# Performance work log

Measured on AMD Instinct MI355X. Metric: run time of the kernel, lower is better.

Reference implementation:

```python
import jax, jax.numpy as jnp
import numpy as np

B, T = 16, 2048
D_MODEL, D_INNER, D_STATE, D_CONV, DT_RANK = 64, 128, 16, 4, 4

def leaky(x):
    return jnp.where(x >= 0, x, 0.01 * x)

def silu(x):
    return x * jax.nn.sigmoid(x)

def conv1d(x, w, b, pad):
    # x: (b,c,t), w: (o,i,k)
    y = jax.lax.conv_general_dilated(x, w, (1,), [(pad, pad)],
        dimension_numbers=('NCH', 'OIH', 'NCH'))
    return y + b[None, :, None]

def pixel_shuffle_1d(x, r):
    b, cr, t = x.shape
    c = cr // r
    return x.reshape(b, c, r, t).transpose(0, 1, 3, 2).reshape(b, c, t * r)

def rmsnorm(x, w, eps=1e-5):
    return x * jax.lax.rsqrt(jnp.mean(x * x, -1, keepdims=True) + eps) * w

def batchnorm(x, g, b, eps=1e-5):
    # training-mode BatchNorm1d: stats over (N, T) per channel
    mu = jnp.mean(x, axis=(0, 2), keepdims=True)
    var = jnp.var(x, axis=(0, 2), keepdims=True)
    return (x - mu) * jax.lax.rsqrt(var + eps) * g[None, :, None] + b[None, :, None]

def selective_scan(u, delta, A, Bm, Cm, D):
    # u, delta: (b,t,d); Bm, Cm: (b,t,n); A: (d,n); D: (d,)
    def step(h, inp):
        d_t, u_t, B_t, C_t = inp  # (b,d),(b,d),(b,n),(b,n)
        dA = jnp.exp(d_t[:, :, None] * A[None])              # (b,d,n)
        h = h * dA + (d_t * u_t)[:, :, None] * B_t[:, None, :]
        y = jnp.einsum('bdn,bn->bd', h, C_t)
        return h, y
    h0 = jnp.zeros((u.shape[0], A.shape[0], A.shape[1]), u.dtype)
    xs = tuple(jnp.swapaxes(a, 0, 1) for a in (delta, u, Bm, Cm))
    _, ys = jax.lax.scan(step, h0, xs)
    return jnp.swapaxes(ys, 0, 1) + u * D[None, None, :]

def mamba_layer(x, norm_w, in_proj_w, dwconv_w, dwconv_b, x_proj_w,
                dt_proj_w, dt_proj_b, A_log, D, out_proj_w):
    # x: (b,t,d_model); pre-norm residual Mamba block
    xn = rmsnorm(x, norm_w)
    xz = xn @ in_proj_w.T                                    # (b,t,2*d_inner)
    xm, z = jnp.split(xz, 2, axis=-1)
    # causal depthwise conv over time (pad left d_conv-1)
    xc = jax.lax.conv_general_dilated(jnp.swapaxes(xm, 1, 2), dwconv_w,
        (1,), [(D_CONV - 1, 0)], dimension_numbers=('NCH', 'OIH', 'NCH'),
        feature_group_count=D_INNER) + dwconv_b[None, :, None]
    xm = silu(jnp.swapaxes(xc, 1, 2))                        # (b,t,d_inner)
    x_dbl = xm @ x_proj_w.T                                  # (b,t,dt_rank+2n)
    dt, Bm, Cm = jnp.split(x_dbl, [DT_RANK, DT_RANK + D_STATE], axis=-1)
    delta = jax.nn.softplus(dt @ dt_proj_w.T + dt_proj_b)    # (b,t,d_inner)
    A = -jnp.exp(A_log)                                      # (d_inner,n)
    y = selective_scan(xm, delta, A, Bm, Cm, D)
    y = y * silu(z)
    return x + y @ out_proj_w.T

def setup_inputs():
    key = jax.random.key(0)
    ks = jax.random.split(key, 16)
    p = lambda k, shp, s=0.02: jax.random.normal(k, shp, jnp.float32) * s
    return {
        'x': jax.random.normal(ks[0], (B, 12, T), jnp.float32),
        'conv_in_w': p(ks[1], (D_MODEL, 12, 15)), 'conv_in_b': jnp.zeros((D_MODEL,), jnp.float32),
        'norm_w': jnp.ones((D_MODEL,), jnp.float32),
        'in_proj_w': p(ks[2], (2 * D_INNER, D_MODEL)),
        'dwconv_w': p(ks[3], (D_INNER, 1, D_CONV), 0.2), 'dwconv_b': jnp.zeros((D_INNER,), jnp.float32),
        'x_proj_w': p(ks[4], (DT_RANK + 2 * D_STATE, D_INNER)),
        'dt_proj_w': p(ks[5], (D_INNER, DT_RANK), 0.5),
        'dt_proj_b': jnp.full((D_INNER,), -2.0, jnp.float32),
        'A_log': jnp.tile(jnp.log(jnp.arange(1, D_STATE + 1, dtype=jnp.float32))[None], (D_INNER, 1)),
        'D': jnp.ones((D_INNER,), jnp.float32),
        'out_proj_w': p(ks[6], (D_MODEL, D_INNER)),
        'merge_w': p(ks[7], (D_MODEL, D_MODEL, 15)), 'merge_b': jnp.zeros((D_MODEL,), jnp.float32),
        'bn_g': jnp.ones((D_MODEL,), jnp.float32), 'bn_b': jnp.zeros((D_MODEL,), jnp.float32),
        'up1_w': p(ks[8], (320 * 5, D_MODEL, 15)), 'up1_b': jnp.zeros((320 * 5,), jnp.float32),
        'up2_w': p(ks[9], (128 * 2, 320, 15)), 'up2_b': jnp.zeros((128 * 2,), jnp.float32),
        'out_w': p(ks[10], (12, 128, 15)), 'out_b': jnp.zeros((12,), jnp.float32),
    }

def reference(x, conv_in_w, conv_in_b, norm_w, in_proj_w, dwconv_w, dwconv_b,
              x_proj_w, dt_proj_w, dt_proj_b, A_log, D, out_proj_w,
              merge_w, merge_b, bn_g, bn_b, up1_w, up1_b, up2_w, up2_b,
              out_w, out_b):
    h = leaky(conv1d(x, conv_in_w, conv_in_b, 7))            # (b,64,t)
    hold = h
    s = mamba_layer(jnp.swapaxes(h, 1, 2), norm_w, in_proj_w, dwconv_w,
                    dwconv_b, x_proj_w, dt_proj_w, dt_proj_b, A_log, D,
                    out_proj_w)
    h2 = jnp.swapaxes(s, 1, 2)                               # (b,64,t)
    m = batchnorm(conv1d(h2, merge_w, merge_b, 7), bn_g, bn_b) + hold
    u5 = leaky(pixel_shuffle_1d(conv1d(m, up1_w, up1_b, 7), 5))    # (b,320,5t)
    u10 = leaky(pixel_shuffle_1d(conv1d(u5, up2_w, up2_b, 7), 2))  # (b,128,10t)
    return conv1d(u10, out_w, out_b, 7)                      # (b,12,10t)
```

## Files before the change

### kernel.cpp

```cpp
#include <hip/hip_runtime.h>
#include <hip/hip_bf16.h>
#include <math.h>

typedef __hip_bfloat16 bf16;
typedef __attribute__((ext_vector_type(8))) short short8;
typedef __attribute__((ext_vector_type(4))) float f32x4;

#define BB 16
#define TT 2048
#define DM 64
#define DI 128
#define DSN 16
#define NCHK 32
#define CLEN 64

union U8 { int4 i4; unsigned short u[8]; };

__device__ __forceinline__ bf16  f2b(float v){ return __float2bfloat16(v); }
__device__ __forceinline__ float b2f(bf16 v){ return __bfloat162float(v); }
__device__ __forceinline__ unsigned short f2bu(float v){
  bf16 b = __float2bfloat16(v); unsigned short u; __builtin_memcpy(&u,&b,2); return u;
}
__device__ __forceinline__ float bu2f(unsigned short u){
  unsigned int x = ((unsigned int)u) << 16; float f; __builtin_memcpy(&f,&x,4); return f;
}
__device__ __forceinline__ float siluf(float x){ return x / (1.f + __expf(-x)); }
__device__ __forceinline__ float leakyf(float x){ return x >= 0.f ? x : 0.01f*x; }
__device__ __forceinline__ float softplusf(float x){ return x > 20.f ? x : log1pf(__expf(x)); }

__global__ __launch_bounds__(256) void k_zero(float* __restrict__ p, int n){
  int i = blockIdx.x*256 + threadIdx.x;
  if (i < n) p[i] = 0.f;
}

__global__ __launch_bounds__(256) void k_pack(
    const float* __restrict__ w, short* __restrict__ wp,
    int COUT, int CIN, int NTg, int NCH, int NTAP)
{
  int i = blockIdx.x*256 + threadIdx.x;
  int lane = i & 63, frag = i >> 6;
  int total = NTAP*NCH*NTg;
  if (frag >= total) return;
  int cot = frag % NTg; int kc = frag / NTg;
  int ch = kc % NCH;    int k  = kc / NCH;
  int co = cot*16 + (lane & 15);
  int ci0 = ch*32 + (lane >> 4)*8;
  unsigned short v[8];
  #pragma unroll
  for (int j = 0; j < 8; j++)
    v[j] = (co < COUT) ? f2bu(w[((size_t)co*CIN + ci0 + j)*NTAP + k]) : (unsigned short)0;
  short* dst = wp + (size_t)frag*512 + lane*8;
  *(int4*)dst = *(int4*)v;
}

__global__ __launch_bounds__(256) void k_conv_in(
    const float* __restrict__ x, const float* __restrict__ w,
    const float* __restrict__ bias, float* __restrict__ h, bf16* __restrict__ ht)
{
  __shared__ float sx[12][272];
  __shared__ float sw[12][15];
  int tid = threadIdx.x;
  int t0 = blockIdx.x * 256;
  int co = blockIdx.y;
  int b  = blockIdx.z;
  for (int i = tid; i < 12*15; i += 256) sw[i/15][i%15] = w[co*180 + i];
  for (int i = tid; i < 12*270; i += 256) {
    int ci = i/270, L = i%270;
    int tt = t0 - 7 + L;
    sx[ci][L] = (tt >= 0 && tt < TT) ? x[((size_t)b*12+ci)*TT + tt] : 0.f;
  }
  __syncthreads();
  float acc = bias[co];
  #pragma unroll
  for (int ci = 0; ci < 12; ci++) {
    #pragma unroll
    for (int k = 0; k < 15; k++)
      acc += sx[ci][tid+k]*sw[ci][k];
  }
  acc = leakyf(acc);
  int t = t0 + tid;
  h [((size_t)b*DM + co)*TT + t] = acc;
  ht[((size_t)b*TT + t)*DM + co] = f2b(acc);
}

__global__ __launch_bounds__(256) void k_inproj_mfma(
    const bf16* __restrict__ ht, const float* __restrict__ nw,
    const short* __restrict__ wp, bf16* __restrict__ xm, bf16* __restrict__ z)
{
  __shared__ short sxa[64*128];
  __shared__ float sred[64][4];
  const int tid = threadIdx.x;
  const int lane = tid & 63, wv = tid >> 6;
  const int lnm = lane & 15, quad = lane >> 4;
  const size_t bt0 = (size_t)blockIdx.x * 64;

  {
    int row = tid >> 2, part = tid & 3, ch0 = part*16;
    const short* src = (const short*)ht + (bt0 + row)*64 + ch0;
    U8 p0, p1; p0.i4 = *(const int4*)src; p1.i4 = *(const int4*)(src + 8);
    float f[16]; float ss = 0.f;
    #pragma unroll
    for (int j = 0; j < 8; j++) { f[j] = bu2f(p0.u[j]); f[8+j] = bu2f(p1.u[j]); }
    #pragma unroll
    for (int j = 0; j < 16; j++) ss += f[j]*f[j];
    sred[row][part] = ss;
    __syncthreads();
    float tot = sred[row][0]+sred[row][1]+sred[row][2]+sred[row][3];
    float sc = rsqrtf(tot*(1.f/64.f) + 1e-5f);
    U8 o0, o1;
    #pragma unroll
    for (int j = 0; j < 8; j++) {
      o0.u[j] = f2bu(f[j]  *sc*nw[ch0+j]);
      o1.u[j] = f2bu(f[8+j]*sc*nw[ch0+8+j]);
    }
    int s0 = part*2, s1 = part*2+1;
    *(int4*)(sxa + row*128 + ((s0 ^ (row&7))<<3)) = o0.i4;
    *(int4*)(sxa + row*128 + ((s1 ^ (row&7))<<3)) = o1.i4;
  }
  __syncthreads();

  f32x4 acc[4][4];
  #pragma unroll
  for (int m = 0; m < 4; m++)
    #pragma unroll
    for (int n = 0; n < 4; n++) acc[m][n] = (f32x4){0.f,0.f,0.f,0.f};

  #pragma unroll
  for (int kc = 0; kc < 2; kc++) {
    short8 bfr[4];
    #pragma unroll
    for (int n = 0; n < 4; n++) {
      int fid = kc*16 + wv*4 + n;
      bfr[n] = *(const short8*)(wp + (size_t)fid*512 + lane*8);
    }
    #pragma unroll
    for (int m = 0; m < 4; m++) {
      int r2 = m*16 + lnm;
      short8 a = *(const short8*)(sxa + r2*128 + (((kc*4+quad) ^ (r2&7))<<3));
      #pragma unroll
      for (int n = 0; n < 4; n++)
        acc[m][n] = __builtin_amdgcn_mfma_f32_16x16x32_bf16(a, bfr[n], acc[m][n], 0, 0, 0);
    }
  }

  #pragma unroll
  for (int m = 0; m < 4; m++)
    #pragma unroll
    for (int n = 0; n < 4; n++) {
      int co = wv*64 + n*16 + lnm;
      float v[4] = {acc[m][n].x, acc[m][n].y, acc[m][n].z, acc[m][n].w};
      #pragma unroll
      for (int r = 0; r < 4; r++) {
        size_t t = bt0 + m*16 + quad*4 + r;
        if (co < 128) xm[t*128 + co]       = f2b(v[r]);
        else          z [t*128 + (co-128)] = f2b(v[r]);
      }
    }
}

__global__ __launch_bounds__(256) void k_dwconv(
    const bf16* __restrict__ xm, const float* __restrict__ w,
    const float* __restrict__ bias, float* __restrict__ xcf, bf16* __restrict__ xcb)
{
  int idx = blockIdx.x*256 + threadIdx.x;
  int c = idx & (DI-1);
  int bt = idx >> 7;
  int t = bt & (TT-1);
  float acc = bias[c];
  #pragma unroll
  for (int k = 0; k < 4; k++) {
    int tt = t - 3 + k;
    if (tt >= 0) acc += b2f(xm[(size_t)(bt - 3 + k)*DI + c]) * w[c*4+k];
  }
  float v = siluf(acc);
  xcf[idx] = v;
  xcb[idx] = f2b(v);
}

__global__ __launch_bounds__(256) void k_xproj_mfma(
    const bf16* __restrict__ xcb, const short* __restrict__ wp, float* __restrict__ xd)
{
  __shared__ __align__(16) char smem[256*64];
  const int tid = threadIdx.x;
  const int lane = tid & 63, wv = tid >> 6;
  const int lnm = lane & 15, quad = lane >> 4;
  const size_t bt0 = (size_t)blockIdx.x * 256;
  const int wvt = wv*64;

  f32x4 acc[4][3];
  #pragma unroll
  for (int m = 0; m < 4; m++)
    #pragma unroll
    for (int n = 0; n < 3; n++) acc[m][n] = (f32x4){0.f,0.f,0.f,0.f};

  for (int ch = 0; ch < 4; ch++) {
    __syncthreads();
    int sl = tid & 3;
    for (int r = tid >> 2; r < 256; r += 64) {
      int4 v = *(const int4*)((const short*)xcb + (bt0 + r)*128 + ch*32 + sl*8);
      *(int4*)(&smem[r*64 + ((sl ^ (r & 3)) << 4)]) = v;
    }
    __syncthreads();
    short8 bfr[3];
    #pragma unroll
    for (int n = 0; n < 3; n++)
      bfr[n] = *(const short8*)(wp + (size_t)(ch*3+n)*512 + lane*8);
    #pragma unroll
    for (int m = 0; m < 4; m++) {
      int row = wvt + m*16 + lnm;
      short8 a = *(const short8*)(&smem[row*64 + ((quad ^ (row & 3)) << 4)]);
      #pragma unroll
      for (int n = 0; n < 3; n++)
        acc[m][n] = __builtin_amdgcn_mfma_f32_16x16x32_bf16(a, bfr[n], acc[m][n], 0, 0, 0);
    }
  }
  #pragma unroll
  for (int m = 0; m < 4; m++)
    #pragma unroll
    for (int n = 0; n < 3; n++) {
      int cho = n*16 + lnm;
      float v[4] = {acc[m][n].x, acc[m][n].y, acc[m][n].z, acc[m][n].w};
      #pragma unroll
      for (int r = 0; r < 4; r++) {
        size_t t = bt0 + wvt + m*16 + quad*4 + r;
        xd[t*48 + cho] = v[r];
      }
    }
}

__global__ __launch_bounds__(256) void k_delta(
    const float* __restrict__ xd, const float* __restrict__ w,
    const float* __restrict__ bias, float* __restrict__ dlt)
{
  int idx = blockIdx.x*256 + threadIdx.x;
  int c = idx & (DI-1);
  int bt = idx >> 7;
  const float* dt = xd + (size_t)bt*48;
  float acc = bias[c];
  #pragma unroll
  for (int r = 0; r < 4; r++) acc += dt[r]*w[c*4+r];
  dlt[idx] = softplusf(acc);
}

__global__ __launch_bounds__(256) void k_scan_sum(
    const float* __restrict__ dlt, const float* __restrict__ xcf,
    const float* __restrict__ xd, const float* __restrict__ A_log,
    float* __restrict__ gP, float* __restrict__ gS)
{
  int tid = threadIdx.x;
  int n = tid & 15, dl = tid >> 4;
  int d = blockIdx.x*16 + dl;
  int b = blockIdx.y, ck = blockIdx.z;
  float A = -__expf(A_log[d*DSN + n]);
  float P = 1.f, h = 0.f;
  size_t base = (size_t)b*TT + (size_t)ck*CLEN;
  for (int i = 0; i < CLEN; i++) {
    size_t ib = base + i;
    float dd = dlt[ib*DI + d];
    float uu = xcf[ib*DI + d];
    float Bv = xd [ib*48 + 4 + n];
    float dA = __expf(dd*A);
    h = h*dA + dd*uu*Bv;
    P *= dA;
  }
  size_t idx = (((size_t)b*NCHK + ck)*DI + d)*DSN + n;
  gP[idx] = P; gS[idx] = h;
}

__global__ __launch_bounds__(256) void k_scan_comb(
    const float* __restrict__ gP, const float* __restrict__ gS,
    float* __restrict__ ghs)
{
  int idx = blockIdx.x*256 + threadIdx.x;
  int n = idx & 15, d = (idx >> 4) & 127, b = idx >> 11;
  float h = 0.f;
  for (int c = 0; c < NCHK; c++) {
    size_t j = (((size_t)b*NCHK + c)*DI + d)*DSN + n;
    ghs[j] = h;
    h = gP[j]*h + gS[j];
  }
}

__global__ __launch_bounds__(256) void k_scan_out(
    const float* __restrict__ dlt, const float* __restrict__ xcf,
    const float* __restrict__ xd, const float* __restrict__ A_log,
    const float* __restrict__ Dv, const float* __restrict__ ghs,
    float* __restrict__ y)
{
  int tid = threadIdx.x;
  int n = tid & 15, dl = tid >> 4;
  int d = blockIdx.x*16 + dl;
  int b = blockIdx.y, ck = blockIdx.z;
  float A = -__expf(A_log[d*DSN + n]);
  float Dd = Dv[d];
  size_t idx = (((size_t)b*NCHK + ck)*DI + d)*DSN + n;
  float h = ghs[idx];
  size_t base = (size_t)b*TT + (size_t)ck*CLEN;
  for (int i = 0; i < CLEN; i++) {
    size_t ib = base + i;
    float dd = dlt[ib*DI + d];
    float uu = xcf[ib*DI + d];
    float Bv = xd [ib*48 + 4  + n];
    float Cv = xd [ib*48 + 20 + n];
    float dA = __expf(dd*A);
    h = h*dA + dd*uu*Bv;
    float c = h*Cv;
    c += __shfl_xor(c, 1); c += __shfl_xor(c, 2);
    c += __shfl_xor(c, 4); c += __shfl_xor(c, 8);
    if (n == 0) y[ib*DI + d] = c + uu*Dd;
  }
}

__global__ __launch_bounds__(256) void k_outproj_mfma(
    const float* __restrict__ gy, const bf16* __restrict__ gz,
    const bf16* __restrict__ ht, const short* __restrict__ wp,
    bf16* __restrict__ st)
{
  __shared__ __align__(16) char smem[256*64];
  const int tid = threadIdx.x;
  const int lane = tid & 63, wv = tid >> 6;
  const int lnm = lane & 15, quad = lane >> 4;
  const size_t bt0 = (size_t)blockIdx.x * 256;
  const int wvt = wv*64;

  f32x4 acc[4][4];
  #pragma unroll
  for (int m = 0; m < 4; m++)
    #pragma unroll
    for (int n = 0; n < 4; n++) acc[m][n] = (f32x4){0.f,0.f,0.f,0.f};

  for (int ch = 0; ch < 4; ch++) {
    __syncthreads();
    int sl = tid & 3;
    for (int r = tid >> 2; r < 256; r += 64) {
      size_t base = (bt0 + r)*(size_t)DI + ch*32 + sl*8;
      float4 y0 = *(const float4*)(gy + base);
      float4 y1 = *(const float4*)(gy + base + 4);
      U8 zz; zz.i4 = *(const int4*)((const short*)gz + base);
      float yv[8] = {y0.x, y0.y, y0.z, y0.w, y1.x, y1.y, y1.z, y1.w};
      U8 o;
      #pragma unroll
      for (int j = 0; j < 8; j++)
        o.u[j] = f2bu(yv[j] * siluf(bu2f(zz.u[j])));
      *(int4*)(&smem[r*64 + ((sl ^ (r & 3)) << 4)]) = o.i4;
    }
    __syncthreads();
    short8 bfr[4];
    #pragma unroll
    for (int n = 0; n < 4; n++)
      bfr[n] = *(const short8*)(wp + (size_t)(ch*4+n)*512 + lane*8);
    #pragma unroll
    for (int m = 0; m < 4; m++) {
      int row = wvt + m*16 + lnm;
      short8 a = *(const short8*)(&smem[row*64 + ((quad ^ (row & 3)) << 4)]);
      #pragma unroll
      for (int n = 0; n < 4; n++)
        acc[m][n] = __builtin_amdgcn_mfma_f32_16x16x32_bf16(a, bfr[n], acc[m][n], 0, 0, 0);
    }
  }
  #pragma unroll
  for (int m = 0; m < 4; m++)
    #pragma unroll
    for (int n = 0; n < 4; n++) {
      int cho = n*16 + lnm;
      float v[4] = {acc[m][n].x, acc[m][n].y, acc[m][n].z, acc[m][n].w};
      #pragma unroll
      for (int r = 0; r < 4; r++) {
        size_t t = bt0 + wvt + m*16 + quad*4 + r;
        st[t*DM + cho] = f2b(v[r] + b2f(ht[t*DM + cho]));
      }
    }
}

template<int CIN, int NSUB, int R, bool LEAKY, bool STATS, int OUTMODE>
__global__ __launch_bounds__(256) void mfma_conv(
    const bf16* __restrict__ inp, const short* __restrict__ wp,
    const float* __restrict__ bias, void* __restrict__ outv,
    float* __restrict__ stats, int Tlen, int NTg)
{
  constexpr int NCH = CIN/32;
  constexpr int NC  = 16*NSUB;
  constexpr int NCR = NC/R;
  constexpr int STAGE_B = 270*64;
  constexpr int EPI_B = (OUTMODE==0) ? 4*64*NC*2 : 4*16*68*4;
  constexpr int LDSB = (STAGE_B > EPI_B) ? STAGE_B : EPI_B;
  __shared__ __align__(16) char smem[LDSB];

  const int tid  = threadIdx.x;
  const int lane = tid & 63;
  const int wv   = tid >> 6;
  const int lnm  = lane & 15;
  const int quad = lane >> 4;
  const int t0   = blockIdx.x * 256;
  const int by   = blockIdx.y;
  const int b    = blockIdx.z;
  const int wvt  = wv*64;

  f32x4 acc[4][NSUB];
  #pragma unroll
  for (int m = 0; m < 4; m++)
    #pragma unroll
    for (int n = 0; n < NSUB; n++)
      acc[m][n] = (f32x4){0.f,0.f,0.f,0.f};

  for (int ch = 0; ch < NCH; ch++) {
    __syncthreads();
    {
      int sl = tid & 3;
      for (int r = tid >> 2; r < 270; r += 64) {
        int t = t0 - 7 + r;
        int4 v = {0,0,0,0};
        if (t >= 0 && t < Tlen)
          v = *(const int4*)(inp + ((size_t)((size_t)b*Tlen + t))*CIN + ch*32 + sl*8);
        *(int4*)(&smem[r*64 + ((sl ^ (r & 3)) << 4)]) = v;
      }
    }
    __syncthreads();

    short8 bcur[NSUB], bnxt[NSUB];
    #pragma unroll
    for (int n = 0; n < NSUB; n++) {
      size_t fid = (size_t)((0*NCH + ch)*NTg + by*NSUB + n);
      bcur[n] = *(const short8*)(wp + fid*512 + lane*8);
    }
    for (int k = 0; k < 15; k++) {
      if (k < 14) {
        #pragma unroll
        for (int n = 0; n < NSUB; n++) {
          size_t fid = (size_t)(((k+1)*NCH + ch)*NTg + by*NSUB + n);
          bnxt[n] = *(const short8*)(wp + fid*512 + lane*8);
        }
      }
      short8 af[4];
      #pragma unroll
      for (int m = 0; m < 4; m++) {
        int row = wvt + m*16 + lnm + k;
        af[m] = *(const short8*)(&smem[row*64 + ((quad ^ (row & 3)) << 4)]);
      }
      #pragma unroll
      for (int m = 0; m < 4; m++)
        #pragma unroll
        for (int n = 0; n < NSUB; n++)
          acc[m][n] = __builtin_amdgcn_mfma_f32_16x16x32_bf16(af[m], bcur[n], acc[m][n], 0, 0, 0);
      #pragma unroll
      for (int n = 0; n < NSUB; n++) bcur[n] = bnxt[n];
    }
  }

  #pragma unroll
  for (int n = 0; n < NSUB; n++) {
    float bv = bias[by*NC + n*16 + lnm];
    #pragma unroll
    for (int m = 0; m < 4; m++) {
      acc[m][n].x += bv; acc[m][n].y += bv; acc[m][n].z += bv; acc[m][n].w += bv;
    }
  }
  if (STATS) {
    #pragma unroll
    for (int n = 0; n < NSUB; n++) {
      float s1 = 0.f, s2 = 0.f;
      #pragma unroll
      for (int m = 0; m < 4; m++) {
        f32x4 a = acc[m][n];
        s1 += a.x + a.y + a.z + a.w;
        s2 += a.x*a.x + a.y*a.y + a.z*a.z + a.w*a.w;
      }
      s1 += __shfl_xor(s1, 16); s1 += __shfl_xor(s1, 32);
      s2 += __shfl_xor(s2, 16); s2 += __shfl_xor(s2, 32);
      if (quad == 0) {
        atomicAdd(&stats[by*NC + n*16 + lnm], s1);
        atomicAdd(&stats[64 + by*NC + n*16 + lnm], s2);
      }
    }
  }
  if (LEAKY) {
    #pragma unroll
    for (int m = 0; m < 4; m++)
      #pragma unroll
      for (int n = 0; n < NSUB; n++) {
        acc[m][n].x = leakyf(acc[m][n].x); acc[m][n].y = leakyf(acc[m][n].y);
        acc[m][n].z = leakyf(acc[m][n].z); acc[m][n].w = leakyf(acc[m][n].w);
      }
  }

  __syncthreads();

  if (OUTMODE == 0) {
    short* Cw = (short*)smem + wv*64*NC;
    #pragma unroll
    for (int m = 0; m < 4; m++)
      #pragma unroll
      for (int n = 0; n < NSUB; n++) {
        int co = n*16 + lnm;
        int p = co % R, c = co / R;
        float vv[4] = {acc[m][n].x, acc[m][n].y, acc[m][n].z, acc[m][n].w};
        #pragma unroll
        for (int r = 0; r < 4; r++) {
          int t = m*16 + quad*4 + r;
          Cw[t*NC + p*NCR + c] = (short)f2bu(vv[r]);
        }
      }
    const int SPT = NC/8;
    const int CTOT = NTg*16/R;
    bf16* outp = (bf16*)outv;
    size_t brow = (size_t)b * ((size_t)Tlen*R);
    for (int j = lane; j < 64*SPT; j += 64) {
      int t = j / SPT, sl = j % SPT;
      int cosw = sl*8;
      int p = cosw / NCR, csl = cosw % NCR;
      int tout = (t0 + wvt + t)*R + p;
      size_t ga = (brow + tout)*(size_t)CTOT + (size_t)by*NCR + csl;
      *(int4*)((short*)outp + ga) = *(const int4*)(Cw + t*NC + cosw);
    }
  } else {
    float* Cw = (float*)smem + wv*(16*68);
    #pragma unroll
    for (int m = 0; m < 4; m++) {
      float vv[4] = {acc[m][0].x, acc[m][0].y, acc[m][0].z, acc[m][0].w};
      #pragma unroll
      for (int r = 0; r < 4; r++) {
        int t = m*16 + quad*4 + r;
        Cw[lnm*68 + t] = vv[r];
      }
    }
    float* outf = (float*)outv;
    for (int j = lane; j < 12*16; j += 64) {
      int co = j >> 4, t4 = (j & 15)*4;
      size_t ga = ((size_t)b*12 + co)*(size_t)Tlen + t0 + wvt + t4;
      *(float4*)(outf + ga) = *(const float4*)(Cw + co*68 + t4);
    }
  }
}

__global__ __launch_bounds__(256) void k_bnadd2(
    const bf16* __restrict__ m2, const float* __restrict__ stats,
    const float* __restrict__ g, const float* __restrict__ bb,
    const float* __restrict__ h, bf16* __restrict__ mt)
{
  int idx = blockIdx.x*256 + threadIdx.x;
  int c = idx & 63;
  int t = (idx >> 6) & (TT-1);
  int b = idx >> 17;
  const float cnt = (float)(BB*TT);
  float mu  = stats[c] / cnt;
  float var = stats[64+c] / cnt - mu*mu;
  float inv = rsqrtf(var + 1e-5f);
  float v = b2f(m2[idx]);
  float hv = h[((size_t)b*64 + c)*TT + t];
  mt[idx] = f2b((v - mu)*inv*g[c] + bb[c] + hv);
}

extern "C" void kernel_launch(void* const* d_in, const int* in_sizes, int n_in,
                              void* d_out, int out_size, void* d_ws, size_t ws_size,
                              hipStream_t stream)
{
  const float* in_x       = (const float*)d_in[0];
  const float* conv_in_w  = (const float*)d_in[1];
  const float* conv_in_b  = (const float*)d_in[2];
  const float* norm_w     = (const float*)d_in[3];
  const float* in_proj_w  = (const float*)d_in[4];
  const float* dwconv_w   = (const float*)d_in[5];
  const float* dwconv_b   = (const float*)d_in[6];
  const float* x_proj_w   = (const float*)d_in[7];
  const float* dt_proj_w  = (const float*)d_in[8];
  const float* dt_proj_b  = (const float*)d_in[9];
  const float* A_log      = (const float*)d_in[10];
  const float* Dvec       = (const float*)d_in[11];
  const float* out_proj_w = (const float*)d_in[12];
  const float* merge_w    = (const float*)d_in[13];
  const float* merge_b    = (const float*)d_in[14];
  const float* bn_g       = (const float*)d_in[15];
  const float* bn_b       = (const float*)d_in[16];
  const float* up1_w      = (const float*)d_in[17];
  const float* up1_b      = (const float*)d_in[18];
  const float* up2_w      = (const float*)d_in[19];
  const float* up2_b      = (const float*)d_in[20];
  const float* out_w      = (const float*)d_in[21];
  const float* out_b      = (const float*)d_in[22];
  float* out = (float*)d_out;

  size_t off = 0;
  auto take = [&](size_t bytes) -> void* {
    void* p = (char*)d_ws + off;
    off += (bytes + 255) & ~(size_t)255;
    return p;
  };
  const size_t F_BDMT = (size_t)BB*DM*TT;
  const size_t F_BTDI = (size_t)BB*TT*DI;
  float* g_h   = (float*)take(F_BDMT*4);
  bf16*  g_ht  = (bf16*) take(F_BDMT*2);
  bf16*  g_st  = (bf16*) take(F_BDMT*2);
  bf16*  g_m2  = (bf16*) take(F_BDMT*2);
  bf16*  g_mt  = (bf16*) take(F_BDMT*2);
  float* g_stt = (float*)take(512);
  short* wp_mg = (short*)take((size_t)15*2*4 *512*2);
  short* wp_u1 = (short*)take((size_t)15*2*100*512*2);
  short* wp_u2 = (short*)take((size_t)15*10*16*512*2);
  short* wp_oc = (short*)take((size_t)15*4*1  *512*2);
  short* wp_ip = (short*)take((size_t)1*2*16*512*2);
  short* wp_xp = (short*)take((size_t)1*4*3 *512*2);
  short* wp_op = (short*)take((size_t)1*4*4 *512*2);
  size_t mamba_base = off;
  bf16*  g_xm  = (bf16*) take(F_BTDI*2);
  bf16*  g_z   = (bf16*) take(F_BTDI*2);
  float* g_xcf = (float*)take(F_BTDI*4);
  bf16*  g_xcb = (bf16*) take(F_BTDI*2);
  float* g_xd  = (float*)take((size_t)BB*TT*48*4);
  float* g_dl  = (float*)take(F_BTDI*4);
  float* g_y   = (float*)take(F_BTDI*4);
  float* g_P   = (float*)take((size_t)BB*NCHK*DI*DSN*4);
  float* g_S   = (float*)take((size_t)BB*NCHK*DI*DSN*4);
  float* g_hs  = (float*)take((size_t)BB*NCHK*DI*DSN*4);
  bf16*  g_u10 = (bf16*)((char*)d_ws + mamba_base);
  bf16*  g_u5  = (bf16*)take((size_t)BB*10240*320*2);
  if (off > ws_size) return;

  k_zero<<<1, 256, 0, stream>>>(g_stt, 128);
  k_pack<<<(15*2*4*64+255)/256, 256, 0, stream>>>(merge_w, wp_mg, 64, 64, 4, 2, 15);
  k_pack<<<(15*2*100*64+255)/256, 256, 0, stream>>>(up1_w, wp_u1, 1600, 64, 100, 2, 15);
  k_pack<<<(15*10*16*64+255)/256, 256, 0, stream>>>(up2_w, wp_u2, 256, 320, 16, 10, 15);
  k_pack<<<(15*4*1*64+255)/256, 256, 0, stream>>>(out_w, wp_oc, 12, 128, 1, 4, 15);
  k_pack<<<(1*2*16*64+255)/256, 256, 0, stream>>>(in_proj_w, wp_ip, 256, 64, 16, 2, 1);
  k_pack<<<(1*4*3*64+255)/256, 256, 0, stream>>>(x_proj_w, wp_xp, 36, 128, 3, 4, 1);
  k_pack<<<(1*4*4*64+255)/256, 256, 0, stream>>>(out_proj_w, wp_op, 64, 128, 4, 4, 1);

  k_conv_in<<<dim3(TT/256, DM, BB), 256, 0, stream>>>(in_x, conv_in_w, conv_in_b, g_h, g_ht);

  k_inproj_mfma<<<BB*TT/64, 256, 0, stream>>>(g_ht, norm_w, wp_ip, g_xm, g_z);
  k_dwconv<<<BB*TT*DI/256, 256, 0, stream>>>(g_xm, dwconv_w, dwconv_b, g_xcf, g_xcb);
  k_xproj_mfma<<<BB*TT/256, 256, 0, stream>>>(g_xcb, wp_xp, g_xd);
  k_delta<<<BB*TT*DI/256, 256, 0, stream>>>(g_xd, dt_proj_w, dt_proj_b, g_dl);
  k_scan_sum<<<dim3(DI/16, BB, NCHK), 256, 0, stream>>>(g_dl, g_xcf, g_xd, A_log, g_P, g_S);
  k_scan_comb<<<BB*DI*DSN/256, 256, 0, stream>>>(g_P, g_S, g_hs);
  k_scan_out<<<dim3(DI/16, BB, NCHK), 256, 0, stream>>>(g_dl, g_xcf, g_xd, A_log, Dvec, g_hs, g_y);
  k_outproj_mfma<<<BB*TT/256, 256, 0, stream>>>(g_y, g_z, g_ht, wp_op, g_st);

  mfma_conv<64,4,1,false,true,0><<<dim3(TT/256, 1, BB), 256, 0, stream>>>(
      g_st, wp_mg, merge_b, g_m2, g_stt, TT, 4);
  k_bnadd2<<<BB*TT*64/256, 256, 0, stream>>>(g_m2, g_stt, bn_g, bn_b, g_h, g_mt);

  mfma_conv<64,5,5,true,false,0><<<dim3(TT/256, 20, BB), 256, 0, stream>>>(
      g_mt, wp_u1, up1_b, g_u5, nullptr, TT, 100);

  mfma_conv<320,4,2,true,false,0><<<dim3(TT*5/256, 4, BB), 256, 0, stream>>>(
      g_u5, wp_u2, up2_b, g_u10, nullptr, TT*5, 16);

  mfma_conv<128,1,1,false,false,1><<<dim3(TT*10/256, 1, BB), 256, 0, stream>>>(
      g_u10, wp_oc, out_b, out, nullptr, TT*10, 1);
}
```

Baseline: 889.2 us.

## Drop fp32 intermediates, widen conv LDS staging to 64 channels, double up2 N-tile

Removes the fp32 copies of the conv_in output and the dwconv output. The residual, the scan inputs and the scan output y are now read and written as bf16, which cuts global memory traffic across several Mamba kernels. The generic MFMA conv now stages 64 input channels per LDS pass with an 8-way swizzle, and it drops the register double-buffering of weight fragments. The up2 conv uses NSUB=8 with half as many grid blocks, and the epilogue is split into halves so the LDS budget holds. This adds bf16 rounding of the residual and of y, and the larger per-wave accumulator set may raise register pressure.

```diff
diff --git a/kernel.cpp b/kernel.cpp
--- a/kernel.cpp
+++ b/kernel.cpp
@@ -55,7 +55,7 @@
 
 __global__ __launch_bounds__(256) void k_conv_in(
     const float* __restrict__ x, const float* __restrict__ w,
-    const float* __restrict__ bias, float* __restrict__ h, bf16* __restrict__ ht)
+    const float* __restrict__ bias, bf16* __restrict__ ht)
 {
   __shared__ float sx[12][272];
   __shared__ float sw[12][15];
@@ -79,7 +79,6 @@
   }
   acc = leakyf(acc);
   int t = t0 + tid;
-  h [((size_t)b*DM + co)*TT + t] = acc;
   ht[((size_t)b*TT + t)*DM + co] = f2b(acc);
 }
 
@@ -160,7 +159,7 @@
 
 __global__ __launch_bounds__(256) void k_dwconv(
     const bf16* __restrict__ xm, const float* __restrict__ w,
-    const float* __restrict__ bias, float* __restrict__ xcf, bf16* __restrict__ xcb)
+    const float* __restrict__ bias, bf16* __restrict__ xcb)
 {
   int idx = blockIdx.x*256 + threadIdx.x;
   int c = idx & (DI-1);
@@ -172,9 +171,7 @@
     int tt = t - 3 + k;
     if (tt >= 0) acc += b2f(xm[(size_t)(bt - 3 + k)*DI + c]) * w[c*4+k];
   }
-  float v = siluf(acc);
-  xcf[idx] = v;
-  xcb[idx] = f2b(v);
+  xcb[idx] = f2b(siluf(acc));
 }
 
 __global__ __launch_bounds__(256) void k_xproj_mfma(
@@ -243,7 +240,7 @@
 }
 
 __global__ __launch_bounds__(256) void k_scan_sum(
-    const float* __restrict__ dlt, const float* __restrict__ xcf,
+    const float* __restrict__ dlt, const bf16* __restrict__ xcb,
     const float* __restrict__ xd, const float* __restrict__ A_log,
     float* __restrict__ gP, float* __restrict__ gS)
 {
@@ -257,7 +254,7 @@
   for (int i = 0; i < CLEN; i++) {
     size_t ib = base + i;
     float dd = dlt[ib*DI + d];
-    float uu = xcf[ib*DI + d];
+    float uu = b2f(xcb[ib*DI + d]);
     float Bv = xd [ib*48 + 4 + n];
     float dA = __expf(dd*A);
     h = h*dA + dd*uu*Bv;
@@ -282,10 +279,10 @@
 }
 
 __global__ __launch_bounds__(256) void k_scan_out(
-    const float* __restrict__ dlt, const float* __restrict__ xcf,
+    const float* __restrict__ dlt, const bf16* __restrict__ xcb,
     const float* __restrict__ xd, const float* __restrict__ A_log,
     const float* __restrict__ Dv, const float* __restrict__ ghs,
-    float* __restrict__ y)
+    bf16* __restrict__ y)
 {
   int tid = threadIdx.x;
   int n = tid & 15, dl = tid >> 4;
@@ -299,7 +296,7 @@
   for (int i = 0; i < CLEN; i++) {
     size_t ib = base + i;
     float dd = dlt[ib*DI + d];
-    float uu = xcf[ib*DI + d];
+    float uu = b2f(xcb[ib*DI + d]);
     float Bv = xd [ib*48 + 4  + n];
     float Cv = xd [ib*48 + 20 + n];
     float dA = __expf(dd*A);
@@ -307,12 +304,12 @@
     float c = h*Cv;
     c += __shfl_xor(c, 1); c += __shfl_xor(c, 2);
     c += __shfl_xor(c, 4); c += __shfl_xor(c, 8);
-    if (n == 0) y[ib*DI + d] = c + uu*Dd;
+    if (n == 0) y[ib*DI + d] = f2b(c + uu*Dd);
   }
 }
 
 __global__ __launch_bounds__(256) void k_outproj_mfma(
-    const float* __restrict__ gy, const bf16* __restrict__ gz,
+    const bf16* __restrict__ gy, const bf16* __restrict__ gz,
     const bf16* __restrict__ ht, const short* __restrict__ wp,
     bf16* __restrict__ st)
 {
@@ -334,14 +331,12 @@
     int sl = tid & 3;
     for (int r = tid >> 2; r < 256; r += 64) {
       size_t base = (bt0 + r)*(size_t)DI + ch*32 + sl*8;
-      float4 y0 = *(const float4*)(gy + base);
-      float4 y1 = *(const float4*)(gy + base + 4);
+      U8 yy; yy.i4 = *(const int4*)((const short*)gy + base);
       U8 zz; zz.i4 = *(const int4*)((const short*)gz + base);
-      float yv[8] = {y0.x, y0.y, y0.z, y0.w, y1.x, y1.y, y1.z, y1.w};
       U8 o;
       #pragma unroll
       for (int j = 0; j < 8; j++)
-        o.u[j] = f2bu(yv[j] * siluf(bu2f(zz.u[j])));
+        o.u[j] = f2bu(bu2f(yy.u[j]) * siluf(bu2f(zz.u[j])));
       *(int4*)(&smem[r*64 + ((sl ^ (r & 3)) << 4)]) = o.i4;
     }
     __syncthreads();
@@ -378,11 +373,16 @@
     const float* __restrict__ bias, void* __restrict__ outv,
     float* __restrict__ stats, int Tlen, int NTg)
 {
-  constexpr int NCH = CIN/32;
-  constexpr int NC  = 16*NSUB;
-  constexpr int NCR = NC/R;
-  constexpr int STAGE_B = 270*64;
-  constexpr int EPI_B = (OUTMODE==0) ? 4*64*NC*2 : 4*16*68*4;
+  constexpr int NCH64 = CIN/64;
+  constexpr int NCH32 = CIN/32;
+  constexpr int NC   = 16*NSUB;
+  constexpr int NCR  = NC/R;
+  constexpr int NHALF = (NC > 80) ? 2 : 1;
+  constexpr int NCh  = NC/NHALF;
+  constexpr int NCRh = NCR/NHALF;
+  constexpr int NSUBh = NSUB/NHALF;
+  constexpr int STAGE_B = 270*128;
+  constexpr int EPI_B = (OUTMODE==0) ? 4*64*NCh*2 : 4*16*68*4;
   constexpr int LDSB = (STAGE_B > EPI_B) ? STAGE_B : EPI_B;
   __shared__ __align__(16) char smem[LDSB];
 
@@ -403,47 +403,39 @@
     for (int n = 0; n < NSUB; n++)
       acc[m][n] = (f32x4){0.f,0.f,0.f,0.f};
 
-  for (int ch = 0; ch < NCH; ch++) {
+  for (int ch = 0; ch < NCH64; ch++) {
     __syncthreads();
-    {
-      int sl = tid & 3;
-      for (int r = tid >> 2; r < 270; r += 64) {
-        int t = t0 - 7 + r;
-        int4 v = {0,0,0,0};
-        if (t >= 0 && t < Tlen)
-          v = *(const int4*)(inp + ((size_t)((size_t)b*Tlen + t))*CIN + ch*32 + sl*8);
-        *(int4*)(&smem[r*64 + ((sl ^ (r & 3)) << 4)]) = v;
-      }
+    for (int i = tid; i < 270*8; i += 256) {
+      int r = i >> 3, sl = i & 7;
+      int t = t0 - 7 + r;
+      int4 v = {0,0,0,0};
+      if (t >= 0 && t < Tlen)
+        v = *(const int4*)(inp + ((size_t)b*Tlen + t)*CIN + ch*64 + sl*8);
+      *(int4*)(&smem[r*128 + ((sl ^ (r & 7)) << 4)]) = v;
     }
     __syncthreads();
 
-    short8 bcur[NSUB], bnxt[NSUB];
-    #pragma unroll
-    for (int n = 0; n < NSUB; n++) {
-      size_t fid = (size_t)((0*NCH + ch)*NTg + by*NSUB + n);
-      bcur[n] = *(const short8*)(wp + fid*512 + lane*8);
-    }
     for (int k = 0; k < 15; k++) {
-      if (k < 14) {
+      #pragma unroll
+      for (int c2 = 0; c2 < 2; c2++) {
+        short8 bfr[NSUB];
         #pragma unroll
         for (int n = 0; n < NSUB; n++) {
-          size_t fid = (size_t)(((k+1)*NCH + ch)*NTg + by*NSUB + n);
-          bnxt[n] = *(const short8*)(wp + fid*512 + lane*8);
+          size_t fid = (size_t)((k*NCH32 + ch*2 + c2)*NTg + by*NSUB + n);
+          bfr[n] = *(const short8*)(wp + fid*512 + lane*8);
         }
-      }
-      short8 af[4];
-      #pragma unroll
-      for (int m = 0; m < 4; m++) {
-        int row = wvt + m*16 + lnm + k;
-        af[m] = *(const short8*)(&smem[row*64 + ((quad ^ (row & 3)) << 4)]);
-      }
-      #pragma unroll
-      for (int m = 0; m < 4; m++)
+        short8 af[4];
         #pragma unroll
-        for (int n = 0; n < NSUB; n++)
-          acc[m][n] = __builtin_amdgcn_mfma_f32_16x16x32_bf16(af[m], bcur[n], acc[m][n], 0, 0, 0);
-      #pragma unroll
-      for (int n = 0; n < NSUB; n++) bcur[n] = bnxt[n];
+        for (int m = 0; m < 4; m++) {
+          int row = wvt + m*16 + lnm + k;
+          af[m] = *(const short8*)(&smem[row*128 + (((c2*4+quad) ^ (row & 7)) << 4)]);
+        }
+        #pragma unroll
+        for (int m = 0; m < 4; m++)
+          #pragma unroll
+          for (int n = 0; n < NSUB; n++)
+            acc[m][n] = __builtin_amdgcn_mfma_f32_16x16x32_bf16(af[m], bfr[n], acc[m][n], 0, 0, 0);
+      }
     }
   }
 
@@ -486,31 +478,35 @@
   __syncthreads();
 
   if (OUTMODE == 0) {
-    short* Cw = (short*)smem + wv*64*NC;
-    #pragma unroll
-    for (int m = 0; m < 4; m++)
-      #pragma unroll
-      for (int n = 0; n < NSUB; n++) {
-        int co = n*16 + lnm;
-        int p = co % R, c = co / R;
-        float vv[4] = {acc[m][n].x, acc[m][n].y, acc[m][n].z, acc[m][n].w};
-        #pragma unroll
-        for (int r = 0; r < 4; r++) {
-          int t = m*16 + quad*4 + r;
-          Cw[t*NC + p*NCR + c] = (short)f2bu(vv[r]);
-        }
-      }
-    const int SPT = NC/8;
     const int CTOT = NTg*16/R;
     bf16* outp = (bf16*)outv;
     size_t brow = (size_t)b * ((size_t)Tlen*R);
-    for (int j = lane; j < 64*SPT; j += 64) {
-      int t = j / SPT, sl = j % SPT;
-      int cosw = sl*8;
-      int p = cosw / NCR, csl = cosw % NCR;
-      int tout = (t0 + wvt + t)*R + p;
-      size_t ga = (brow + tout)*(size_t)CTOT + (size_t)by*NCR + csl;
-      *(int4*)((short*)outp + ga) = *(const int4*)(Cw + t*NC + cosw);
+    #pragma unroll
+    for (int h = 0; h < NHALF; h++) {
+      short* Cw = (short*)smem + wv*64*NCh;
+      #pragma unroll
+      for (int m = 0; m < 4; m++)
+        #pragma unroll
+        for (int nn = 0; nn < NSUBh; nn++) {
+          int n = h*NSUBh + nn;
+          int cof = n*16 + lnm;
+          int p = cof % R, c = cof / R;
+          float vv[4] = {acc[m][n].x, acc[m][n].y, acc[m][n].z, acc[m][n].w};
+          #pragma unroll
+          for (int r = 0; r < 4; r++) {
+            int t = m*16 + quad*4 + r;
+            Cw[t*NCh + p*NCRh + (c - h*NCRh)] = (short)f2bu(vv[r]);
+          }
+        }
+      const int SPT = NCh/8;
+      for (int j = lane; j < 64*SPT; j += 64) {
+        int t = j / SPT, sl = j % SPT;
+        int cosw = sl*8;
+        int p = cosw / NCRh, coff = cosw % NCRh;
+        int tout = (t0 + wvt + t)*R + p;
+        size_t ga = (brow + tout)*(size_t)CTOT + (size_t)by*NCR + h*NCRh + coff;
+        *(int4*)((short*)outp + ga) = *(const int4*)(Cw + t*NCh + cosw);
+      }
     }
   } else {
     float* Cw = (float*)smem + wv*(16*68);
@@ -535,19 +531,16 @@
 __global__ __launch_bounds__(256) void k_bnadd2(
     const bf16* __restrict__ m2, const float* __restrict__ stats,
     const float* __restrict__ g, const float* __restrict__ bb,
-    const float* __restrict__ h, bf16* __restrict__ mt)
+    const bf16* __restrict__ ht, bf16* __restrict__ mt)
 {
   int idx = blockIdx.x*256 + threadIdx.x;
   int c = idx & 63;
-  int t = (idx >> 6) & (TT-1);
-  int b = idx >> 17;
   const float cnt = (float)(BB*TT);
   float mu  = stats[c] / cnt;
   float var = stats[64+c] / cnt - mu*mu;
   float inv = rsqrtf(var + 1e-5f);
   float v = b2f(m2[idx]);
-  float hv = h[((size_t)b*64 + c)*TT + t];
-  mt[idx] = f2b((v - mu)*inv*g[c] + bb[c] + hv);
+  mt[idx] = f2b((v - mu)*inv*g[c] + bb[c] + b2f(ht[idx]));
 }
 
 extern "C" void kernel_launch(void* const* d_in, const int* in_sizes, int n_in,
@@ -587,7 +580,6 @@
   };
   const size_t F_BDMT = (size_t)BB*DM*TT;
   const size_t F_BTDI = (size_t)BB*TT*DI;
-  float* g_h   = (float*)take(F_BDMT*4);
   bf16*  g_ht  = (bf16*) take(F_BDMT*2);
   bf16*  g_st  = (bf16*) take(F_BDMT*2);
   bf16*  g_m2  = (bf16*) take(F_BDMT*2);
@@ -603,14 +595,15 @@
   size_t mamba_base = off;
   bf16*  g_xm  = (bf16*) take(F_BTDI*2);
   bf16*  g_z   = (bf16*) take(F_BTDI*2);
-  float* g_xcf = (float*)take(F_BTDI*4);
   bf16*  g_xcb = (bf16*) take(F_BTDI*2);
   float* g_xd  = (float*)take((size_t)BB*TT*48*4);
   float* g_dl  = (float*)take(F_BTDI*4);
-  float* g_y   = (float*)take(F_BTDI*4);
+  bf16*  g_y   = (bf16*) take(F_BTDI*2);
   float* g_P   = (float*)take((size_t)BB*NCHK*DI*DSN*4);
   float* g_S   = (float*)take((size_t)BB*NCHK*DI*DSN*4);
   float* g_hs  = (float*)take((size_t)BB*NCHK*DI*DSN*4);
+  const size_t U10_B = (size_t)BB*20480*128*2;
+  if (off < mamba_base + U10_B) off = mamba_base + U10_B;
   bf16*  g_u10 = (bf16*)((char*)d_ws + mamba_base);
   bf16*  g_u5  = (bf16*)take((size_t)BB*10240*320*2);
   if (off > ws_size) return;
@@ -624,25 +617,25 @@
   k_pack<<<(1*4*3*64+255)/256, 256, 0, stream>>>(x_proj_w, wp_xp, 36, 128, 3, 4, 1);
   k_pack<<<(1*4*4*64+255)/256, 256, 0, stream>>>(out_proj_w, wp_op, 64, 128, 4, 4, 1);
 
-  k_conv_in<<<dim3(TT/256, DM, BB), 256, 0, stream>>>(in_x, conv_in_w, conv_in_b, g_h, g_ht);
+  k_conv_in<<<dim3(TT/256, DM, BB), 256, 0, stream>>>(in_x, conv_in_w, conv_in_b, g_ht);
 
   k_inproj_mfma<<<BB*TT/64, 256, 0, stream>>>(g_ht, norm_w, wp_ip, g_xm, g_z);
-  k_dwconv<<<BB*TT*DI/256, 256, 0, stream>>>(g_xm, dwconv_w, dwconv_b, g_xcf, g_xcb);
+  k_dwconv<<<BB*TT*DI/256, 256, 0, stream>>>(g_xm, dwconv_w, dwconv_b, g_xcb);
   k_xproj_mfma<<<BB*TT/256, 256, 0, stream>>>(g_xcb, wp_xp, g_xd);
   k_delta<<<BB*TT*DI/256, 256, 0, stream>>>(g_xd, dt_proj_w, dt_proj_b, g_dl);
-  k_scan_sum<<<dim3(DI/16, BB, NCHK), 256, 0, stream>>>(g_dl, g_xcf, g_xd, A_log, g_P, g_S);
+  k_scan_sum<<<dim3(DI/16, BB, NCHK), 256, 0, stream>>>(g_dl, g_xcb, g_xd, A_log, g_P, g_S);
   k_scan_comb<<<BB*DI*DSN/256, 256, 0, stream>>>(g_P, g_S, g_hs);
-  k_scan_out<<<dim3(DI/16, BB, NCHK), 256, 0, stream>>>(g_dl, g_xcf, g_xd, A_log, Dvec, g_hs, g_y);
+  k_scan_out<<<dim3(DI/16, BB, NCHK), 256, 0, stream>>>(g_dl, g_xcb, g_xd, A_log, Dvec, g_hs, g_y);
   k_outproj_mfma<<<BB*TT/256, 256, 0, stream>>>(g_y, g_z, g_ht, wp_op, g_st);
 
   mfma_conv<64,4,1,false,true,0><<<dim3(TT/256, 1, BB), 256, 0, stream>>>(
       g_st, wp_mg, merge_b, g_m2, g_stt, TT, 4);
-  k_bnadd2<<<BB*TT*64/256, 256, 0, stream>>>(g_m2, g_stt, bn_g, bn_b, g_h, g_mt);
+  k_bnadd2<<<BB*TT*64/256, 256, 0, stream>>>(g_m2, g_stt, bn_g, bn_b, g_ht, g_mt);
 
   mfma_conv<64,5,5,true,false,0><<<dim3(TT/256, 20, BB), 256, 0, stream>>>(
       g_mt, wp_u1, up1_b, g_u5, nullptr, TT, 100);
 
-  mfma_conv<320,4,2,true,false,0><<<dim3(TT*5/256, 4, BB), 256, 0, stream>>>(
+  mfma_conv<320,8,2,true,false,0><<<dim3(TT*5/256, 2, BB), 256, 0, stream>>>(
       g_u5, wp_u2, up2_b, g_u10, nullptr, TT*5, 16);
 
   mfma_conv<128,1,1,false,false,1><<<dim3(TT*10/256, 1, BB), 256, 0, stream>>>(
```

Result: slower. 1.147 ms (+29.0%).
